# Performance work log

Measured on AMD Instinct MI355X. Metric: run time of the kernel, lower is better.

The kernel has to match this reference:

```python
import jax, jax.numpy as jnp
import numpy as np

B, K, D = 128, 32, 1024
E = 32
H = int(D * 0.25)  # d_hidden = d_block * moe_ratio


def _rsqrt_uniform(key, shape, d):
    bound = d ** -0.5
    return jax.random.uniform(key, shape, jnp.float32, -bound, bound)


def setup_inputs() -> dict:
    key = jax.random.key(0)
    ks = jax.random.split(key, 7)
    return {
        "x": jax.random.normal(ks[0], (B, K, D), jnp.float32),
        "router_w": _rsqrt_uniform(ks[1], (E, D), D),   # nn.Linear(d_block, num_experts).weight
        "router_b": _rsqrt_uniform(ks[2], (E,), D),
        "weights1": _rsqrt_uniform(ks[3], (E, D, H), H),
        "bias1": _rsqrt_uniform(ks[4], (E, H), H),
        "weights2": _rsqrt_uniform(ks[5], (E, H, D), D),
        "bias2": _rsqrt_uniform(ks[6], (E, D), D),
    }


def reference(x, router_w, router_b, weights1, bias1, weights2, bias2):
    b, k, d = x.shape
    x_flat = x.reshape(-1, d)                      # [N, D], N = B*K
    n = x_flat.shape[0]
    # top-1 router (argmax of logits, like torch.argmax)
    logits = x_flat @ router_w.T + router_b        # [N, E]
    routed_idx = jnp.argmax(logits, axis=-1)       # [N]

    # Each expert is a 2-layer MLP; note the original applies act1 (ReLU)
    # after BOTH layers, and dropout=0.0 is an identity.
    def expert_mlp(w1, b1, w2, b2):
        h = jax.nn.relu(x_flat @ w1 + b1)          # [N, H]
        return jax.nn.relu(h @ w2 + b2)            # [N, D]

    y_all = jax.vmap(expert_mlp)(weights1, bias1, weights2, bias2)  # [E, N, D]
    out_flat = y_all[routed_idx, jnp.arange(n)]    # select routed expert per token
    return out_flat.reshape(b, k, d)
```

## Files before the change

### kernel.cpp

```cpp
#include <hip/hip_runtime.h>


#define N_TOK 4096
#define DDIM  1024
#define HDIM  256
#define NEXP  32
#define TPX   136

typedef __attribute__((ext_vector_type(8))) short bf16x8;
typedef __attribute__((ext_vector_type(4))) float f32x4;

__device__ __forceinline__ unsigned short f2bf(float f) {
  union { float f; unsigned u; } v; v.f = f;
  unsigned r = v.u + 0x7FFFu + ((v.u >> 16) & 1u);
  return (unsigned short)(r >> 16);
}
__device__ __forceinline__ float bf2f(unsigned short h) {
  union { unsigned u; float f; } v; v.u = ((unsigned)h) << 16;
  return v.f;
}
__device__ __forceinline__ int swz(int row, int kk) {
  return row * 72 + (kk ^ (((row >> 3) & 7) << 3));
}

__global__ __launch_bounds__(256) void router_kernel(
    const float* __restrict__ x, const float* __restrict__ rw,
    const float* __restrict__ rb, int* __restrict__ routed) {
  __shared__ float red[4][64][8];
  int b = blockIdx.x;
  int t = threadIdx.x, w = t >> 6, l = t & 63;
  int m = l & 15, kb = l >> 4;
  int tok = b * 16 + m;
  int kbase = w * 256;
  const float* xrow = x + (size_t)tok * DDIM + kbase + kb * 8;
  const float* w0p  = rw + (size_t)m * DDIM + kbase + kb * 8;
  const float* w1p  = rw + (size_t)(16 + m) * DDIM + kbase + kb * 8;
  f32x4 acc0 = {0.f,0.f,0.f,0.f}, acc1 = {0.f,0.f,0.f,0.f};
#pragma unroll
  for (int q = 0; q < 8; q++) {
    float4 xa = *(const float4*)(xrow + q * 32);
    float4 xc = *(const float4*)(xrow + q * 32 + 4);
    float4 wa0 = *(const float4*)(w0p + q * 32);
    float4 wc0 = *(const float4*)(w0p + q * 32 + 4);
    float4 wa1 = *(const float4*)(w1p + q * 32);
    float4 wc1 = *(const float4*)(w1p + q * 32 + 4);
    float xv[8]  = {xa.x, xa.y, xa.z, xa.w, xc.x, xc.y, xc.z, xc.w};
    float wv0[8] = {wa0.x, wa0.y, wa0.z, wa0.w, wc0.x, wc0.y, wc0.z, wc0.w};
    float wv1[8] = {wa1.x, wa1.y, wa1.z, wa1.w, wc1.x, wc1.y, wc1.z, wc1.w};
    bf16x8 xhi, xlo, h0, l0, h1, l1;
#pragma unroll
    for (int i = 0; i < 8; i++) {
      unsigned short hh;
      hh = f2bf(xv[i]);  xhi[i] = (short)hh; xlo[i] = (short)f2bf(xv[i]  - bf2f(hh));
      hh = f2bf(wv0[i]); h0[i]  = (short)hh; l0[i]  = (short)f2bf(wv0[i] - bf2f(hh));
      hh = f2bf(wv1[i]); h1[i]  = (short)hh; l1[i]  = (short)f2bf(wv1[i] - bf2f(hh));
    }
    acc0 = __builtin_amdgcn_mfma_f32_16x16x32_bf16(xhi, h0, acc0, 0, 0, 0);
    acc0 = __builtin_amdgcn_mfma_f32_16x16x32_bf16(xlo, h0, acc0, 0, 0, 0);
    acc0 = __builtin_amdgcn_mfma_f32_16x16x32_bf16(xhi, l0, acc0, 0, 0, 0);
    acc0 = __builtin_amdgcn_mfma_f32_16x16x32_bf16(xlo, l0, acc0, 0, 0, 0);
    acc1 = __builtin_amdgcn_mfma_f32_16x16x32_bf16(xhi, h1, acc1, 0, 0, 0);
    acc1 = __builtin_amdgcn_mfma_f32_16x16x32_bf16(xlo, h1, acc1, 0, 0, 0);
    acc1 = __builtin_amdgcn_mfma_f32_16x16x32_bf16(xhi, l1, acc1, 0, 0, 0);
    acc1 = __builtin_amdgcn_mfma_f32_16x16x32_bf16(xlo, l1, acc1, 0, 0, 0);
  }
  *(f32x4*)&red[w][l][0] = acc0;
  *(f32x4*)&red[w][l][4] = acc1;
  __syncthreads();
  if (w == 0) {
    f32x4 s0 = {0.f,0.f,0.f,0.f}, s1 = {0.f,0.f,0.f,0.f};
#pragma unroll
    for (int ww = 0; ww < 4; ww++) {
      s0 += *(const f32x4*)&red[ww][l][0];
      s1 += *(const f32x4*)&red[ww][l][4];
    }
    float rb0 = rb[m], rb1 = rb[16 + m];
#pragma unroll
    for (int r = 0; r < 4; r++) {
      float v0 = s0[r] + rb0;
      float v1 = s1[r] + rb1;
      float val = v0; int idx = m;
      if (v1 > v0) { val = v1; idx = 16 + m; }
#pragma unroll
      for (int s = 1; s < 16; s <<= 1) {
        float ov = __shfl_xor(val, s);
        int oi = __shfl_xor(idx, s);
        if (ov > val || (ov == val && oi < idx)) { val = ov; idx = oi; }
      }
      if (m == 0) routed[b * 16 + kb * 4 + r] = idx;
    }
  }
}

__global__ __launch_bounds__(512) void scan_scatter_kernel(const int* __restrict__ routed,
    int* __restrict__ meta, int* __restrict__ order) {
  __shared__ int scnt[NEXP];
  __shared__ int scur[NEXP];
  int t = threadIdx.x;
  if (t < NEXP) scnt[t] = 0;
  __syncthreads();
  for (int n = t; n < N_TOK; n += 512) atomicAdd(&scnt[routed[n]], 1);
  __syncthreads();
  if (t < NEXP) {
    int c = scnt[t];
    int nt = (c + 31) >> 5;
    int ic = c;
#pragma unroll
    for (int s = 1; s < NEXP; s <<= 1) {
      int pc = __shfl_up(ic, s);
      if (t >= s) ic += pc;
    }
    int off = ic - c;
    scur[t] = off;
    int cls = t & 7, pos = t >> 3;
    int rank = 0;
#pragma unroll
    for (int j = 0; j < 4; j++) {
      int v = __shfl(nt, cls + j * 8);
      if (pos > j) rank += v;
    }
    for (int s2 = 0; s2 < nt; s2++) {
      int nr = c - s2 * 32; if (nr > 32) nr = 32;
      meta[8 + cls + 8 * (rank + s2)] = (t << 24) | (nr << 16) | (off + s2 * 32);
    }
    if (pos == 3) meta[cls] = rank + nt;
  }
  __syncthreads();
  for (int n = t; n < N_TOK; n += 512) {
    int e = routed[n];
    int p = atomicAdd(&scur[e], 1);
    order[p] = n;
  }
}

template <int KDIM, int NTOT, int COLS, int THREADS, bool A_FP32, bool OUT_BF16>
__global__ __launch_bounds__(THREADS) void expert_gemm_kernel(
    const void* __restrict__ a_src, const float* __restrict__ wsrc,
    const float* __restrict__ bias, const int* __restrict__ meta,
    const int* __restrict__ order, void* __restrict__ outp) {
  constexpr int NCH = KDIM / 64;
  constexpr int NSLAB = NTOT / COLS;
  constexpr int NPASS = (32 * 16) / THREADS;
  __shared__ unsigned short AT[2][32 * 72];
  __shared__ unsigned short BT[2][COLS * 72];
  int bid = blockIdx.x, xcd = bid & 7, r = bid >> 3;
  int ntc = meta[xcd];
  if (r >= ntc * NSLAB) return;
  int y = r / ntc, rank = r - y * ntc;
  int info = meta[8 + xcd + 8 * rank];
  int e = info >> 24, nrow = (info >> 16) & 0xff, ts = info & 0xffff;
  int c0 = y * COLS;
  int t = threadIdx.x, w = t >> 6, l = t & 63, m = l & 15, kb = l >> 4;
  int ak4 = (t & 15) * 4;
  int bcn = t & (COLS - 1), bkg = t / COLS;
  int atrp[NPASS];
  const float* aF[NPASS];
  const unsigned short* aH[NPASS];
#pragma unroll
  for (int pp = 0; pp < NPASS; pp++) {
    atrp[pp] = (t >> 4) + pp * (THREADS >> 4);
    int atok = order[ts + (atrp[pp] < nrow ? atrp[pp] : nrow - 1)];
    aF[pp] = (const float*)a_src + (size_t)atok * KDIM + ak4;
    aH[pp] = (const unsigned short*)a_src + (size_t)atok * KDIM + ak4;
  }
  const float* bS = wsrc + (size_t)e * KDIM * NTOT + c0 + bcn;

  float4 nAf[2][NPASS]; ushort4 nAh[2][NPASS];
  float nB[2][2][8];
  auto LOADC = [&](int c, int rbuf) {
#pragma unroll
    for (int pp = 0; pp < NPASS; pp++) {
      if constexpr (A_FP32) nAf[rbuf][pp] = *(const float4*)(aF[pp] + c * 64);
      else                  nAh[rbuf][pp] = *(const ushort4*)(aH[pp] + c * 64);
    }
#pragma unroll
    for (int u = 0; u < 2; u++)
#pragma unroll
      for (int j = 0; j < 8; j++)
        nB[rbuf][u][j] = bS[(size_t)(c * 64 + (bkg + 4 * u) * 8 + j) * NTOT];
  };

  f32x4 acc0 = {0.f,0.f,0.f,0.f}, acc1 = {0.f,0.f,0.f,0.f};
  LOADC(0, 0);
  LOADC(1, 1);
#pragma unroll
  for (int c = 0; c < NCH; c++) {
    const int p = c & 1;
#pragma unroll
    for (int pp = 0; pp < NPASS; pp++) {
      ushort4 av;
      if constexpr (A_FP32) {
        av.x = f2bf(nAf[p][pp].x); av.y = f2bf(nAf[p][pp].y);
        av.z = f2bf(nAf[p][pp].z); av.w = f2bf(nAf[p][pp].w);
      } else av = nAh[p][pp];
      *(ushort4*)&AT[p][swz(atrp[pp], ak4)] = av;
    }
#pragma unroll
    for (int u = 0; u < 2; u++) {
      bf16x8 pv;
#pragma unroll
      for (int j = 0; j < 8; j++) pv[j] = (short)f2bf(nB[p][u][j]);
      *(bf16x8*)&BT[p][swz(bcn, (bkg + 4 * u) * 8)] = pv;
    }
    if (c + 2 < NCH) LOADC(c + 2, p);
    asm volatile("s_waitcnt lgkmcnt(0)" ::: "memory");
    __builtin_amdgcn_s_barrier();
#pragma unroll
    for (int ks = 0; ks < 2; ks++) {
      int kk = ks * 32 + kb * 8;
      bf16x8 bfr = *(const bf16x8*)&BT[p][swz(w * 16 + m, kk)];
      bf16x8 a0  = *(const bf16x8*)&AT[p][swz(m, kk)];
      bf16x8 a1  = *(const bf16x8*)&AT[p][swz(16 + m, kk)];
      acc0 = __builtin_amdgcn_mfma_f32_16x16x32_bf16(a0, bfr, acc0, 0, 0, 0);
      acc1 = __builtin_amdgcn_mfma_f32_16x16x32_bf16(a1, bfr, acc1, 0, 0, 0);
    }
  }
  int col = c0 + w * 16 + m;
  float bz = bias[e * NTOT + col];
#pragma unroll
  for (int r2 = 0; r2 < 4; r2++) {
    int r0 = kb * 4 + r2;
    if (r0 < nrow) {
      int tok = order[ts + r0];
      float v = acc0[r2] + bz; v = v > 0.f ? v : 0.f;
      if constexpr (OUT_BF16)
        ((unsigned short*)outp)[(size_t)tok * NTOT + col] = f2bf(v);
      else
        ((float*)outp)[(size_t)tok * NTOT + col] = v;
    }
    int r1 = 16 + kb * 4 + r2;
    if (r1 < nrow) {
      int tok = order[ts + r1];
      float v = acc1[r2] + bz; v = v > 0.f ? v : 0.f;
      if constexpr (OUT_BF16)
        ((unsigned short*)outp)[(size_t)tok * NTOT + col] = f2bf(v);
      else
        ((float*)outp)[(size_t)tok * NTOT + col] = v;
    }
  }
}


extern "C" void kernel_launch(void* const* d_in, const int* in_sizes, int n_in,
                              void* d_out, int out_size, void* d_ws, size_t ws_size,
                              hipStream_t stream) {
  const float* x  = (const float*)d_in[0];
  const float* rw = (const float*)d_in[1];
  const float* rb = (const float*)d_in[2];
  const float* w1 = (const float*)d_in[3];
  const float* b1 = (const float*)d_in[4];
  const float* w2 = (const float*)d_in[5];
  const float* b2 = (const float*)d_in[6];
  float* out = (float*)d_out;

  char* ws = (char*)d_ws;
  unsigned short* hb = (unsigned short*)(ws + 0);
  int* routed = (int*)(ws + 2097152);
  int* order  = (int*)(ws + 2113536);
  int* meta   = (int*)(ws + 2129920);

  router_kernel<<<dim3(256), dim3(256), 0, stream>>>(x, rw, rb, routed);
  scan_scatter_kernel<<<dim3(1), dim3(512), 0, stream>>>(routed, meta, order);
  expert_gemm_kernel<DDIM, HDIM, 64, 256, true, true>
      <<<dim3(8 * TPX * (HDIM / 64)), dim3(256), 0, stream>>>(
      x, w1, b1, meta, order, hb);
  expert_gemm_kernel<HDIM, DDIM, 64, 256, false, false>
      <<<dim3(8 * TPX * (DDIM / 64)), dim3(256), 0, stream>>>(
      hb, w2, b2, meta, order, out);
}
```

Baseline: 52.20 us.

## Precompute split-bf16 router weights, emit bf16 x from router, count experts inline

A new prep kernel converts the router weights once per call into hi/lo bf16 arrays and zeroes the expert counters. The router kernel then loads those pre-split weights instead of splitting them per block, writes a bf16 copy of x for the first expert GEMM, and atomically counts tokens per expert. This removes the counting pass from the single-block scan kernel and halves the A-operand bytes the first GEMM reads. In exchange it adds an extra kernel launch and an 8 MB bf16 write of x.

```diff
diff --git a/kernel.cpp b/kernel.cpp
--- a/kernel.cpp
+++ b/kernel.cpp
@@ -23,9 +23,22 @@
   return row * 72 + (kk ^ (((row >> 3) & 7) << 3));
 }
 
+__global__ __launch_bounds__(256) void prep_kernel(const float* __restrict__ rw,
+    unsigned short* __restrict__ rwhi, unsigned short* __restrict__ rwlo,
+    int* __restrict__ counts) {
+  if (blockIdx.x == 0 && threadIdx.x < NEXP) counts[threadIdx.x] = 0;
+  int i = blockIdx.x * 256 + threadIdx.x;
+  float w = rw[i];
+  unsigned short h = f2bf(w);
+  rwhi[i] = h;
+  rwlo[i] = f2bf(w - bf2f(h));
+}
+
 __global__ __launch_bounds__(256) void router_kernel(
-    const float* __restrict__ x, const float* __restrict__ rw,
-    const float* __restrict__ rb, int* __restrict__ routed) {
+    const float* __restrict__ x, const unsigned short* __restrict__ rwhi,
+    const unsigned short* __restrict__ rwlo, const float* __restrict__ rb,
+    unsigned short* __restrict__ xb, int* __restrict__ routed,
+    int* __restrict__ counts) {
   __shared__ float red[4][64][8];
   int b = blockIdx.x;
   int t = threadIdx.x, w = t >> 6, l = t & 63;
@@ -33,36 +46,37 @@
   int tok = b * 16 + m;
   int kbase = w * 256;
   const float* xrow = x + (size_t)tok * DDIM + kbase + kb * 8;
-  const float* w0p  = rw + (size_t)m * DDIM + kbase + kb * 8;
-  const float* w1p  = rw + (size_t)(16 + m) * DDIM + kbase + kb * 8;
+  unsigned short* xbrow = xb + (size_t)tok * DDIM + kbase + kb * 8;
+  const unsigned short* w0h = rwhi + (size_t)m * DDIM + kbase + kb * 8;
+  const unsigned short* w0l = rwlo + (size_t)m * DDIM + kbase + kb * 8;
+  const unsigned short* w1h = rwhi + (size_t)(16 + m) * DDIM + kbase + kb * 8;
+  const unsigned short* w1l = rwlo + (size_t)(16 + m) * DDIM + kbase + kb * 8;
   f32x4 acc0 = {0.f,0.f,0.f,0.f}, acc1 = {0.f,0.f,0.f,0.f};
 #pragma unroll
   for (int q = 0; q < 8; q++) {
     float4 xa = *(const float4*)(xrow + q * 32);
     float4 xc = *(const float4*)(xrow + q * 32 + 4);
-    float4 wa0 = *(const float4*)(w0p + q * 32);
-    float4 wc0 = *(const float4*)(w0p + q * 32 + 4);
-    float4 wa1 = *(const float4*)(w1p + q * 32);
-    float4 wc1 = *(const float4*)(w1p + q * 32 + 4);
-    float xv[8]  = {xa.x, xa.y, xa.z, xa.w, xc.x, xc.y, xc.z, xc.w};
-    float wv0[8] = {wa0.x, wa0.y, wa0.z, wa0.w, wc0.x, wc0.y, wc0.z, wc0.w};
-    float wv1[8] = {wa1.x, wa1.y, wa1.z, wa1.w, wc1.x, wc1.y, wc1.z, wc1.w};
-    bf16x8 xhi, xlo, h0, l0, h1, l1;
+    float xv[8] = {xa.x, xa.y, xa.z, xa.w, xc.x, xc.y, xc.z, xc.w};
+    bf16x8 xhi, xlo;
 #pragma unroll
     for (int i = 0; i < 8; i++) {
-      unsigned short hh;
-      hh = f2bf(xv[i]);  xhi[i] = (short)hh; xlo[i] = (short)f2bf(xv[i]  - bf2f(hh));
-      hh = f2bf(wv0[i]); h0[i]  = (short)hh; l0[i]  = (short)f2bf(wv0[i] - bf2f(hh));
-      hh = f2bf(wv1[i]); h1[i]  = (short)hh; l1[i]  = (short)f2bf(wv1[i] - bf2f(hh));
-    }
-    acc0 = __builtin_amdgcn_mfma_f32_16x16x32_bf16(xhi, h0, acc0, 0, 0, 0);
-    acc0 = __builtin_amdgcn_mfma_f32_16x16x32_bf16(xlo, h0, acc0, 0, 0, 0);
-    acc0 = __builtin_amdgcn_mfma_f32_16x16x32_bf16(xhi, l0, acc0, 0, 0, 0);
-    acc0 = __builtin_amdgcn_mfma_f32_16x16x32_bf16(xlo, l0, acc0, 0, 0, 0);
-    acc1 = __builtin_amdgcn_mfma_f32_16x16x32_bf16(xhi, h1, acc1, 0, 0, 0);
-    acc1 = __builtin_amdgcn_mfma_f32_16x16x32_bf16(xlo, h1, acc1, 0, 0, 0);
-    acc1 = __builtin_amdgcn_mfma_f32_16x16x32_bf16(xhi, l1, acc1, 0, 0, 0);
-    acc1 = __builtin_amdgcn_mfma_f32_16x16x32_bf16(xlo, l1, acc1, 0, 0, 0);
+      unsigned short hh = f2bf(xv[i]);
+      xhi[i] = (short)hh;
+      xlo[i] = (short)f2bf(xv[i] - bf2f(hh));
+    }
+    *(bf16x8*)(xbrow + q * 32) = xhi;
+    bf16x8 wh0 = *(const bf16x8*)(w0h + q * 32);
+    bf16x8 wl0 = *(const bf16x8*)(w0l + q * 32);
+    bf16x8 wh1 = *(const bf16x8*)(w1h + q * 32);
+    bf16x8 wl1 = *(const bf16x8*)(w1l + q * 32);
+    acc0 = __builtin_amdgcn_mfma_f32_16x16x32_bf16(xhi, wh0, acc0, 0, 0, 0);
+    acc0 = __builtin_amdgcn_mfma_f32_16x16x32_bf16(xlo, wh0, acc0, 0, 0, 0);
+    acc0 = __builtin_amdgcn_mfma_f32_16x16x32_bf16(xhi, wl0, acc0, 0, 0, 0);
+    acc1 = __builtin_amdgcn_mfma_f32_16x16x32_bf16(xhi, wh1, acc1, 0, 0, 0);
+    acc1 = __builtin_amdgcn_mfma_f32_16x16x32_bf16(xlo, wh1, acc1, 0, 0, 0);
+    acc1 = __builtin_amdgcn_mfma_f32_16x16x32_bf16(xhi, wl1, acc1, 0, 0, 0);
+    acc0 = __builtin_amdgcn_mfma_f32_16x16x32_bf16(xlo, wl0, acc0, 0, 0, 0);
+    acc1 = __builtin_amdgcn_mfma_f32_16x16x32_bf16(xlo, wl1, acc1, 0, 0, 0);
   }
   *(f32x4*)&red[w][l][0] = acc0;
   *(f32x4*)&red[w][l][4] = acc1;
@@ -87,22 +101,20 @@
         int oi = __shfl_xor(idx, s);
         if (ov > val || (ov == val && oi < idx)) { val = ov; idx = oi; }
       }
-      if (m == 0) routed[b * 16 + kb * 4 + r] = idx;
+      if (m == 0) {
+        routed[b * 16 + kb * 4 + r] = idx;
+        atomicAdd(&counts[idx], 1);
+      }
     }
   }
 }
 
 __global__ __launch_bounds__(512) void scan_scatter_kernel(const int* __restrict__ routed,
-    int* __restrict__ meta, int* __restrict__ order) {
-  __shared__ int scnt[NEXP];
+    const int* __restrict__ counts, int* __restrict__ meta, int* __restrict__ order) {
   __shared__ int scur[NEXP];
   int t = threadIdx.x;
-  if (t < NEXP) scnt[t] = 0;
-  __syncthreads();
-  for (int n = t; n < N_TOK; n += 512) atomicAdd(&scnt[routed[n]], 1);
-  __syncthreads();
   if (t < NEXP) {
-    int c = scnt[t];
+    int c = counts[t];
     int nt = (c + 31) >> 5;
     int ic = c;
 #pragma unroll
@@ -133,46 +145,41 @@
   }
 }
 
-template <int KDIM, int NTOT, int COLS, int THREADS, bool A_FP32, bool OUT_BF16>
-__global__ __launch_bounds__(THREADS) void expert_gemm_kernel(
-    const void* __restrict__ a_src, const float* __restrict__ wsrc,
+template <int KDIM, int NTOT, bool OUT_BF16>
+__global__ __launch_bounds__(256) void expert_gemm_kernel(
+    const unsigned short* __restrict__ a_src, const float* __restrict__ wsrc,
     const float* __restrict__ bias, const int* __restrict__ meta,
     const int* __restrict__ order, void* __restrict__ outp) {
   constexpr int NCH = KDIM / 64;
-  constexpr int NSLAB = NTOT / COLS;
-  constexpr int NPASS = (32 * 16) / THREADS;
+  constexpr int NSLAB = NTOT / 64;
   __shared__ unsigned short AT[2][32 * 72];
-  __shared__ unsigned short BT[2][COLS * 72];
+  __shared__ unsigned short BT[2][64 * 72];
   int bid = blockIdx.x, xcd = bid & 7, r = bid >> 3;
   int ntc = meta[xcd];
   if (r >= ntc * NSLAB) return;
   int y = r / ntc, rank = r - y * ntc;
   int info = meta[8 + xcd + 8 * rank];
   int e = info >> 24, nrow = (info >> 16) & 0xff, ts = info & 0xffff;
-  int c0 = y * COLS;
+  int c0 = y * 64;
   int t = threadIdx.x, w = t >> 6, l = t & 63, m = l & 15, kb = l >> 4;
   int ak4 = (t & 15) * 4;
-  int bcn = t & (COLS - 1), bkg = t / COLS;
-  int atrp[NPASS];
-  const float* aF[NPASS];
-  const unsigned short* aH[NPASS];
-#pragma unroll
-  for (int pp = 0; pp < NPASS; pp++) {
-    atrp[pp] = (t >> 4) + pp * (THREADS >> 4);
+  int bcn = t & 63, bkg = t >> 6;
+  int atrp[2];
+  const unsigned short* aH[2];
+#pragma unroll
+  for (int pp = 0; pp < 2; pp++) {
+    atrp[pp] = (t >> 4) + pp * 16;
     int atok = order[ts + (atrp[pp] < nrow ? atrp[pp] : nrow - 1)];
-    aF[pp] = (const float*)a_src + (size_t)atok * KDIM + ak4;
-    aH[pp] = (const unsigned short*)a_src + (size_t)atok * KDIM + ak4;
+    aH[pp] = a_src + (size_t)atok * KDIM + ak4;
   }
   const float* bS = wsrc + (size_t)e * KDIM * NTOT + c0 + bcn;
 
-  float4 nAf[2][NPASS]; ushort4 nAh[2][NPASS];
+  ushort4 nAh[2][2];
   float nB[2][2][8];
   auto LOADC = [&](int c, int rbuf) {
 #pragma unroll
-    for (int pp = 0; pp < NPASS; pp++) {
-      if constexpr (A_FP32) nAf[rbuf][pp] = *(const float4*)(aF[pp] + c * 64);
-      else                  nAh[rbuf][pp] = *(const ushort4*)(aH[pp] + c * 64);
-    }
+    for (int pp = 0; pp < 2; pp++)
+      nAh[rbuf][pp] = *(const ushort4*)(aH[pp] + c * 64);
 #pragma unroll
     for (int u = 0; u < 2; u++)
 #pragma unroll
@@ -187,14 +194,8 @@
   for (int c = 0; c < NCH; c++) {
     const int p = c & 1;
 #pragma unroll
-    for (int pp = 0; pp < NPASS; pp++) {
-      ushort4 av;
-      if constexpr (A_FP32) {
-        av.x = f2bf(nAf[p][pp].x); av.y = f2bf(nAf[p][pp].y);
-        av.z = f2bf(nAf[p][pp].z); av.w = f2bf(nAf[p][pp].w);
-      } else av = nAh[p][pp];
-      *(ushort4*)&AT[p][swz(atrp[pp], ak4)] = av;
-    }
+    for (int pp = 0; pp < 2; pp++)
+      *(ushort4*)&AT[p][swz(atrp[pp], ak4)] = nAh[p][pp];
 #pragma unroll
     for (int u = 0; u < 2; u++) {
       bf16x8 pv;
@@ -254,17 +255,23 @@
   float* out = (float*)d_out;
 
   char* ws = (char*)d_ws;
-  unsigned short* hb = (unsigned short*)(ws + 0);
-  int* routed = (int*)(ws + 2097152);
-  int* order  = (int*)(ws + 2113536);
-  int* meta   = (int*)(ws + 2129920);
-
-  router_kernel<<<dim3(256), dim3(256), 0, stream>>>(x, rw, rb, routed);
-  scan_scatter_kernel<<<dim3(1), dim3(512), 0, stream>>>(routed, meta, order);
-  expert_gemm_kernel<DDIM, HDIM, 64, 256, true, true>
+  unsigned short* xb   = (unsigned short*)(ws + 0);
+  unsigned short* hb   = (unsigned short*)(ws + 8388608);
+  unsigned short* rwhi = (unsigned short*)(ws + 10485760);
+  unsigned short* rwlo = (unsigned short*)(ws + 10551296);
+  int* routed = (int*)(ws + 10616832);
+  int* order  = (int*)(ws + 10633216);
+  int* counts = (int*)(ws + 10649600);
+  int* meta   = (int*)(ws + 10649728);
+
+  prep_kernel<<<dim3(128), dim3(256), 0, stream>>>(rw, rwhi, rwlo, counts);
+  router_kernel<<<dim3(256), dim3(256), 0, stream>>>(
+      x, rwhi, rwlo, rb, xb, routed, counts);
+  scan_scatter_kernel<<<dim3(1), dim3(512), 0, stream>>>(routed, counts, meta, order);
+  expert_gemm_kernel<DDIM, HDIM, true>
       <<<dim3(8 * TPX * (HDIM / 64)), dim3(256), 0, stream>>>(
-      x, w1, b1, meta, order, hb);
-  expert_gemm_kernel<HDIM, DDIM, 64, 256, false, false>
+      xb, w1, b1, meta, order, hb);
+  expert_gemm_kernel<HDIM, DDIM, false>
       <<<dim3(8 * TPX * (DDIM / 64)), dim3(256), 0, stream>>>(
       hb, w2, b2, meta, order, out);
 }
```

New measurement: 67.85 us. +30.0%, slower.
